# Kernel optimization log

Hardware: AMD Instinct MI355X
Metric: run time of the kernel (lower is better)

## Reference

```python
import jax, jax.numpy as jnp
import numpy as np

HIDDEN_DIM = 512
RADIUS = 128


def rel_pos_indexes(seq_len_q: int, seq_len_k: int, radius: int):
    # (i - j) clamped to [-radius, radius], shifted to [0, 2*radius]
    i = jnp.arange(seq_len_k)[None, :]   # [1, Sk]
    j = jnp.arange(seq_len_q)[:, None]   # [Sq, 1]
    return jnp.clip(i - j, -radius, radius) + radius  # [Sq, Sk] int


def setup_inputs() -> dict:
    key = jax.random.key(0)
    kq, kk, kv, ke = jax.random.split(key, 4)
    B, Sq, Sk, d = 4, 2048, 2048, HIDDEN_DIM
    Q = jax.random.normal(kq, (B, Sq, d), dtype=jnp.float32)
    K = jax.random.normal(kk, (B, Sk, d), dtype=jnp.float32)
    V = jax.random.normal(kv, (B, Sk, d), dtype=jnp.float32)
    # learned relative-position embedding table: (2R+1, d)
    rel_embeds = jax.random.normal(ke, (2 * RADIUS + 1, d), dtype=jnp.float32)
    return {"Q": Q, "K": K, "V": V, "rel_embeds": rel_embeds}


def reference(Q, K, V, rel_embeds):
    B, Sq, d = Q.shape
    Sk = K.shape[1]
    normalizer = jnp.asarray(d ** 0.5, dtype=Q.dtype)
    # content scores: [B, Sq, Sk]
    energy = jnp.einsum('bqd,bkd->bqk', Q, K)
    # relative scores: Q against the (2R+1) relative embeddings -> [B, Sq, 2R+1]
    Q_rel = jnp.einsum('bqd,rd->bqr', Q, rel_embeds)
    idx = rel_pos_indexes(Sq, Sk, RADIUS)  # [Sq, Sk]
    # gather along last dim per query row (same index map for every batch)
    rel_shift = jnp.take_along_axis(Q_rel, idx[None, :, :].repeat(B, axis=0), axis=2)
    energy = (energy + rel_shift) / normalizer
    attn = jax.nn.softmax(energy, axis=2)
    Z = jnp.einsum('bqk,bkd->bqd', attn, V)
    return attn, Z
```

## Files before the change

### kernel.cpp

```cpp
#include <hip/hip_runtime.h>

#define BATCH 4
#define SQL 2048
#define SKL 2048
#define DIM 512
#define NR 257
#define NRP 288
#define RAD 128

typedef __bf16 bf16x8 __attribute__((ext_vector_type(8)));
typedef float f32x4 __attribute__((ext_vector_type(4)));
typedef unsigned short u16;
typedef u16 u16x4 __attribute__((ext_vector_type(4)));
typedef u16 u16x8 __attribute__((ext_vector_type(8)));

__device__ inline u16 f2bf(float x) {
  union { float f; unsigned u; } v; v.f = x;
  unsigned r = v.u + 0x7FFF + ((v.u >> 16) & 1);
  return (u16)(r >> 16);
}

__device__ inline void glds16(const u16* g, const u16* l) {
  __builtin_amdgcn_global_load_lds(
      (const __attribute__((address_space(1))) void*)g,
      (__attribute__((address_space(3))) void*)l, 16, 0, 0);
}

__global__ __launch_bounds__(256) void prep_mem_kernel(const float* __restrict__ Q,
                                                       const float* __restrict__ K,
                                                       const float* __restrict__ V,
                                                       const float* __restrict__ rel,
                                                       u16x4* __restrict__ Qb,
                                                       u16x4* __restrict__ Kb,
                                                       u16* __restrict__ relb,
                                                       u16* __restrict__ Vt) {
  __shared__ float tile[32][33];
  int bid = blockIdx.x, tid = threadIdx.x;
  if (bid < 8192) {
    const f32x4* src = (bid < 4096) ? (const f32x4*)Q : (const f32x4*)K;
    u16x4* dst = (bid < 4096) ? Qb : Kb;
    int i = (bid & 4095) * 256 + tid;
    f32x4 f = src[i];
    u16x4 o;
#pragma unroll
    for (int e = 0; e < 4; e++) o[e] = f2bf(f[e]);
    dst[i] = o;
  } else if (bid < 8768) {
    int i = (bid - 8192) * 256 + tid;
    int r = i >> 9;
    relb[i] = (r < NR) ? f2bf(rel[i]) : (u16)0;
  } else {
    int t = bid - 8768;
    int b = t >> 10, rem = t & 1023;
    int k0 = (rem & 63) * 32, d0 = (rem >> 6) * 32;
    int tx = tid & 31, ty = tid >> 5;
#pragma unroll
    for (int r = 0; r < 4; r++)
      tile[ty + r * 8][tx] = V[((long)b * SKL + k0 + ty + r * 8) * DIM + d0 + tx];
    __syncthreads();
#pragma unroll
    for (int r = 0; r < 4; r++)
      Vt[((long)b * DIM + d0 + ty + r * 8) * SKL + k0 + tx] = f2bf(tile[tx][ty + r * 8]);
  }
}

__global__ __launch_bounds__(256) void qrel_kernel(const u16* __restrict__ Qb,
                                                   const u16* __restrict__ relb,
                                                   float* __restrict__ Qrel) {
  int tid = threadIdx.x;
  int wave = tid >> 6, lane = tid & 63;
  int m0 = blockIdx.x * 64 + wave * 16;
  int j0 = blockIdx.y * 2;
  int fr = lane & 15, fk = (lane >> 4) * 8;
  f32x4 acc[2] = {};
  const u16* qrow = Qb + (long)(m0 + fr) * DIM + fk;
  const u16* r0 = relb + (long)(j0 * 16 + fr) * DIM + fk;
  const u16* r1 = r0 + 16 * DIM;
  for (int k0 = 0; k0 < DIM; k0 += 32) {
    bf16x8 a = *(const bf16x8*)(qrow + k0);
    bf16x8 b0 = *(const bf16x8*)(r0 + k0);
    bf16x8 b1 = *(const bf16x8*)(r1 + k0);
    acc[0] = __builtin_amdgcn_mfma_f32_16x16x32_bf16(a, b0, acc[0], 0, 0, 0);
    acc[1] = __builtin_amdgcn_mfma_f32_16x16x32_bf16(a, b1, acc[1], 0, 0, 0);
  }
  int cr = (lane >> 4) * 4, cc = lane & 15;
#pragma unroll
  for (int t = 0; t < 2; t++)
#pragma unroll
    for (int r = 0; r < 4; r++)
      Qrel[(long)(m0 + cr + r) * NRP + (j0 + t) * 16 + cc] = acc[t][r];
}

__global__ __launch_bounds__(256) void energy_kernel(const u16* __restrict__ Qb,
                                                     const u16* __restrict__ Kb,
                                                     u16* __restrict__ S) {
  int b = blockIdx.z;
  int m0 = blockIdx.y * 128;
  int n0 = blockIdx.x * 128;
  const u16* A = Qb + (long)b * SQL * DIM;
  const u16* Bp = Kb + (long)b * SKL * DIM;
  __shared__ u16 As[128 * 32];
  __shared__ u16 Bs[128 * 32];
  int tid = threadIdx.x;
  int wave = tid >> 6, lane = tid & 63;
  int wm = (wave >> 1) * 64, wn = (wave & 1) * 64;
  int fr = lane & 15, fk = (lane >> 4) * 8;
  int srow = wave * 32 + (lane >> 2);
  int scol = (lane & 3) * 8;
  f32x4 acc[4][4] = {};
  for (int k0 = 0; k0 < DIM; k0 += 32) {
    __syncthreads();
    glds16(A + (long)(m0 + srow) * DIM + k0 + scol, As + (wave * 2 + 0) * 512);
    glds16(A + (long)(m0 + srow + 16) * DIM + k0 + scol, As + (wave * 2 + 1) * 512);
    glds16(Bp + (long)(n0 + srow) * DIM + k0 + scol, Bs + (wave * 2 + 0) * 512);
    glds16(Bp + (long)(n0 + srow + 16) * DIM + k0 + scol, Bs + (wave * 2 + 1) * 512);
    __syncthreads();
    bf16x8 af[4], bfr[4];
#pragma unroll
    for (int i = 0; i < 4; i++) af[i] = *(const bf16x8*)(As + (wm + i * 16 + fr) * 32 + fk);
#pragma unroll
    for (int j = 0; j < 4; j++) bfr[j] = *(const bf16x8*)(Bs + (wn + j * 16 + fr) * 32 + fk);
#pragma unroll
    for (int i = 0; i < 4; i++)
#pragma unroll
      for (int j = 0; j < 4; j++)
        acc[i][j] = __builtin_amdgcn_mfma_f32_16x16x32_bf16(af[i], bfr[j], acc[i][j], 0, 0, 0);
  }
  const float inv_norm = 0.04419417382415922f;
  int cr = (lane >> 4) * 4, cc = lane & 15;
#pragma unroll
  for (int i = 0; i < 4; i++) {
#pragma unroll
    for (int r = 0; r < 4; r++) {
      int q = m0 + wm + i * 16 + cr + r;
      u16* sr = S + ((long)b * SQL + q) * SKL;
#pragma unroll
      for (int j = 0; j < 4; j++)
        sr[n0 + wn + j * 16 + cc] = f2bf(acc[i][j][r] * inv_norm);
    }
  }
}

__global__ __launch_bounds__(256) void softmax_kernel(u16* __restrict__ S,
                                                      const float* __restrict__ Qrel,
                                                      float* __restrict__ attn) {
  long row = blockIdx.x;
  int q = (int)(row & (SQL - 1));
  u16* srow = S + row * SKL;
  float* arow = attn + row * SKL;
  int tid = threadIdx.x;
  int wave = tid >> 6, lane = tid & 63;
  __shared__ float qlds[NR];
  __shared__ float red[4];
  const float inv_norm = 0.04419417382415922f;
  const float* qr = Qrel + row * NRP;
  qlds[tid] = qr[tid] * inv_norm;
  if (tid == 0) qlds[256] = qr[256] * inv_norm;
  bf16x8 v = *(const bf16x8*)(srow + tid * 8);
  __syncthreads();
  float f[8];
  int kb = tid * 8 - q + RAD;
#pragma unroll
  for (int e = 0; e < 8; e++) {
    int idx = kb + e;
    idx = idx < 0 ? 0 : (idx > 2 * RAD ? 2 * RAD : idx);
    f[e] = (float)v[e] + qlds[idx];
  }
  float m = -1e30f;
#pragma unroll
  for (int e = 0; e < 8; e++) m = fmaxf(m, f[e]);
  for (int o = 32; o > 0; o >>= 1) m = fmaxf(m, __shfl_xor(m, o));
  if (lane == 0) red[wave] = m;
  __syncthreads();
  m = fmaxf(fmaxf(red[0], red[1]), fmaxf(red[2], red[3]));
  __syncthreads();
  float s = 0.0f;
  float e8[8];
#pragma unroll
  for (int e = 0; e < 8; e++) { e8[e] = __expf(f[e] - m); s += e8[e]; }
  for (int o = 32; o > 0; o >>= 1) s += __shfl_xor(s, o);
  if (lane == 0) red[wave] = s;
  __syncthreads();
  s = red[0] + red[1] + red[2] + red[3];
  float inv = 1.0f / s;
  f32x4 o0, o1;
  u16x8 pb;
#pragma unroll
  for (int e = 0; e < 4; e++) {
    float p = e8[e] * inv;
    o0[e] = p; pb[e] = f2bf(p);
  }
#pragma unroll
  for (int e = 0; e < 4; e++) {
    float p = e8[e + 4] * inv;
    o1[e] = p; pb[e + 4] = f2bf(p);
  }
  *(f32x4*)(arow + tid * 8) = o0;
  *(f32x4*)(arow + tid * 8 + 4) = o1;
  *(u16x8*)(srow + tid * 8) = pb;
}

__global__ __launch_bounds__(256) void z_kernel(const u16* __restrict__ S,
                                                const u16* __restrict__ Vt,
                                                float* __restrict__ Z) {
  int b = blockIdx.z;
  int m0 = blockIdx.y * 64;
  int n0 = blockIdx.x * 128;
  const u16* A = S + (long)b * SQL * SKL;
  const u16* Bp = Vt + (long)b * DIM * SKL;
  __shared__ u16 As[64 * 32];
  __shared__ u16 Bs[128 * 32];
  int tid = threadIdx.x;
  int wave = tid >> 6, lane = tid & 63;
  int wm = (wave >> 1) * 32, wn = (wave & 1) * 64;
  int fr = lane & 15, fk = (lane >> 4) * 8;
  int srowA = wave * 16 + (lane >> 2);
  int srowB = wave * 32 + (lane >> 2);
  int scol = (lane & 3) * 8;
  f32x4 acc[2][4] = {};
  for (int k0 = 0; k0 < SKL; k0 += 32) {
    __syncthreads();
    glds16(A + (long)(m0 + srowA) * SKL + k0 + scol, As + wave * 512);
    glds16(Bp + (long)(n0 + srowB) * SKL + k0 + scol, Bs + (wave * 2 + 0) * 512);
    glds16(Bp + (long)(n0 + srowB + 16) * SKL + k0 + scol, Bs + (wave * 2 + 1) * 512);
    __syncthreads();
    bf16x8 af[2], bfr[4];
#pragma unroll
    for (int i = 0; i < 2; i++) af[i] = *(const bf16x8*)(As + (wm + i * 16 + fr) * 32 + fk);
#pragma unroll
    for (int j = 0; j < 4; j++) bfr[j] = *(const bf16x8*)(Bs + (wn + j * 16 + fr) * 32 + fk);
#pragma unroll
    for (int i = 0; i < 2; i++)
#pragma unroll
      for (int j = 0; j < 4; j++)
        acc[i][j] = __builtin_amdgcn_mfma_f32_16x16x32_bf16(af[i], bfr[j], acc[i][j], 0, 0, 0);
  }
  int cr = (lane >> 4) * 4, cc = lane & 15;
#pragma unroll
  for (int i = 0; i < 2; i++)
#pragma unroll
    for (int r = 0; r < 4; r++) {
      int q = m0 + wm + i * 16 + cr + r;
      float* zrow = Z + ((long)b * SQL + q) * DIM;
#pragma unroll
      for (int j = 0; j < 4; j++)
        zrow[n0 + wn + j * 16 + cc] = acc[i][j][r];
    }
}


extern "C" void kernel_launch(void* const* d_in, const int* in_sizes, int n_in,
                              void* d_out, int out_size, void* d_ws, size_t ws_size,
                              hipStream_t stream) {
  const float* Q = (const float*)d_in[0];
  const float* K = (const float*)d_in[1];
  const float* V = (const float*)d_in[2];
  const float* rel = (const float*)d_in[3];
  float* attn = (float*)d_out;
  float* Z = attn + (long)BATCH * SQL * SKL;

  char* ws = (char*)d_ws;
  u16* Qb   = (u16*)ws;
  u16* Kb   = (u16*)(ws + 8388608);
  u16* Vt   = (u16*)(ws + 16777216);
  u16* relb = (u16*)(ws + 25165824);
  float* Qrel = (float*)(ws + 25460736);
  u16* S    = (u16*)(ws + 34897920);

  prep_mem_kernel<<<12864, 256, 0, stream>>>(Q, K, V, rel, (u16x4*)Qb, (u16x4*)Kb, relb, Vt);
  qrel_kernel<<<dim3(128, 9), 256, 0, stream>>>(Qb, relb, Qrel);
  energy_kernel<<<dim3(16, 16, BATCH), 256, 0, stream>>>(Qb, Kb, S);
  softmax_kernel<<<8192, 256, 0, stream>>>(S, Qrel, attn);
  z_kernel<<<dim3(4, 32, BATCH), 256, 0, stream>>>(S, Vt, Z);
}
```

Baseline: 239.8 us.

## Double-buffer LDS with XOR-swizzled K=64 tiles in energy and Z GEMMs

Both bf16 GEMM kernels (QK^T energy and attn·V) now stage K-tiles of 64 instead of 32 into two LDS buffers. The next tile is loaded with global_load_lds while the current one is computed, which cuts the syncs per K step and overlaps memory latency with MFMA work. Column chunks are XOR-swizzled by row to avoid LDS bank conflicts on the fragment reads. The cost is much more LDS per block (64KB for energy, 48KB for Z), which may reduce occupancy.

```diff
diff --git a/kernel.cpp b/kernel.cpp
--- a/kernel.cpp
+++ b/kernel.cpp
@@ -99,33 +99,63 @@
   int n0 = blockIdx.x * 128;
   const u16* A = Qb + (long)b * SQL * DIM;
   const u16* Bp = Kb + (long)b * SKL * DIM;
-  __shared__ u16 As[128 * 32];
-  __shared__ u16 Bs[128 * 32];
+  __shared__ u16 lds[32768];
+  u16* As0 = lds;          u16* Bs0 = lds + 8192;
+  u16* As1 = lds + 16384;  u16* Bs1 = lds + 24576;
   int tid = threadIdx.x;
   int wave = tid >> 6, lane = tid & 63;
   int wm = (wave >> 1) * 64, wn = (wave & 1) * 64;
-  int fr = lane & 15, fk = (lane >> 4) * 8;
-  int srow = wave * 32 + (lane >> 2);
-  int scol = (lane & 3) * 8;
+  int fr = lane & 15, g = lane >> 4;
+  int srow = lane >> 3;
+  int scol = ((lane & 7) ^ srow) * 8;
   f32x4 acc[4][4] = {};
-  for (int k0 = 0; k0 < DIM; k0 += 32) {
+
+  auto stage = [&](u16* dA, u16* dB, int k0) {
+#pragma unroll
+    for (int c = 0; c < 4; c++) {
+      int r = wave * 32 + c * 8;
+      glds16(A + (long)(m0 + r + srow) * DIM + k0 + scol, dA + r * 64);
+      glds16(Bp + (long)(n0 + r + srow) * DIM + k0 + scol, dB + r * 64);
+    }
+  };
+  auto compute = [&](const u16* Asb, const u16* Bsb) {
+#pragma unroll
+    for (int s = 0; s < 2; s++) {
+      bf16x8 af[4], bfv[4];
+#pragma unroll
+      for (int i = 0; i < 4; i++) {
+        int row = wm + i * 16 + fr;
+        int cb = (s * 64 + g * 16) ^ ((row & 7) << 4);
+        af[i] = *(const bf16x8*)(Asb + row * 64 + (cb >> 1));
+      }
+#pragma unroll
+      for (int j = 0; j < 4; j++) {
+        int row = wn + j * 16 + fr;
+        int cb = (s * 64 + g * 16) ^ ((row & 7) << 4);
+        bfv[j] = *(const bf16x8*)(Bsb + row * 64 + (cb >> 1));
+      }
+#pragma unroll
+      for (int i = 0; i < 4; i++)
+#pragma unroll
+        for (int j = 0; j < 4; j++)
+          acc[i][j] = __builtin_amdgcn_mfma_f32_16x16x32_bf16(af[i], bfv[j], acc[i][j], 0, 0, 0);
+    }
+  };
+
+  const int NT = DIM / 64;
+  stage(As0, Bs0, 0);
+  __syncthreads();
+  for (int t = 0; t < NT; t += 2) {
+    if (t + 1 < NT) stage(As1, Bs1, (t + 1) * 64);
+    compute(As0, Bs0);
     __syncthreads();
-    glds16(A + (long)(m0 + srow) * DIM + k0 + scol, As + (wave * 2 + 0) * 512);
-    glds16(A + (long)(m0 + srow + 16) * DIM + k0 + scol, As + (wave * 2 + 1) * 512);
-    glds16(Bp + (long)(n0 + srow) * DIM + k0 + scol, Bs + (wave * 2 + 0) * 512);
-    glds16(Bp + (long)(n0 + srow + 16) * DIM + k0 + scol, Bs + (wave * 2 + 1) * 512);
-    __syncthreads();
-    bf16x8 af[4], bfr[4];
-#pragma unroll
-    for (int i = 0; i < 4; i++) af[i] = *(const bf16x8*)(As + (wm + i * 16 + fr) * 32 + fk);
-#pragma unroll
-    for (int j = 0; j < 4; j++) bfr[j] = *(const bf16x8*)(Bs + (wn + j * 16 + fr) * 32 + fk);
-#pragma unroll
-    for (int i = 0; i < 4; i++)
-#pragma unroll
-      for (int j = 0; j < 4; j++)
-        acc[i][j] = __builtin_amdgcn_mfma_f32_16x16x32_bf16(af[i], bfr[j], acc[i][j], 0, 0, 0);
-  }
+    if (t + 1 < NT) {
+      if (t + 2 < NT) stage(As0, Bs0, (t + 2) * 64);
+      compute(As1, Bs1);
+      __syncthreads();
+    }
+  }
+
   const float inv_norm = 0.04419417382415922f;
   int cr = (lane >> 4) * 4, cc = lane & 15;
 #pragma unroll
@@ -208,33 +238,67 @@
   int n0 = blockIdx.x * 128;
   const u16* A = S + (long)b * SQL * SKL;
   const u16* Bp = Vt + (long)b * DIM * SKL;
-  __shared__ u16 As[64 * 32];
-  __shared__ u16 Bs[128 * 32];
+  __shared__ u16 lds[24576];
+  u16* As0 = lds;          u16* Bs0 = lds + 4096;
+  u16* As1 = lds + 12288;  u16* Bs1 = lds + 16384;
   int tid = threadIdx.x;
   int wave = tid >> 6, lane = tid & 63;
   int wm = (wave >> 1) * 32, wn = (wave & 1) * 64;
-  int fr = lane & 15, fk = (lane >> 4) * 8;
-  int srowA = wave * 16 + (lane >> 2);
-  int srowB = wave * 32 + (lane >> 2);
-  int scol = (lane & 3) * 8;
+  int fr = lane & 15, g = lane >> 4;
+  int srow = lane >> 3;
+  int scol = ((lane & 7) ^ srow) * 8;
   f32x4 acc[2][4] = {};
-  for (int k0 = 0; k0 < SKL; k0 += 32) {
+
+  auto stage = [&](u16* dA, u16* dB, int k0) {
+#pragma unroll
+    for (int c = 0; c < 2; c++) {
+      int r = wave * 16 + c * 8;
+      glds16(A + (long)(m0 + r + srow) * SKL + k0 + scol, dA + r * 64);
+    }
+#pragma unroll
+    for (int c = 0; c < 4; c++) {
+      int r = wave * 32 + c * 8;
+      glds16(Bp + (long)(n0 + r + srow) * SKL + k0 + scol, dB + r * 64);
+    }
+  };
+  auto compute = [&](const u16* Asb, const u16* Bsb) {
+#pragma unroll
+    for (int s = 0; s < 2; s++) {
+      bf16x8 af[2], bfv[4];
+#pragma unroll
+      for (int i = 0; i < 2; i++) {
+        int row = wm + i * 16 + fr;
+        int cb = (s * 64 + g * 16) ^ ((row & 7) << 4);
+        af[i] = *(const bf16x8*)(Asb + row * 64 + (cb >> 1));
+      }
+#pragma unroll
+      for (int j = 0; j < 4; j++) {
+        int row = wn + j * 16 + fr;
+        int cb = (s * 64 + g * 16) ^ ((row & 7) << 4);
+        bfv[j] = *(const bf16x8*)(Bsb + row * 64 + (cb >> 1));
+      }
+#pragma unroll
+      for (int i = 0; i < 2; i++)
+#pragma unroll
+        for (int j = 0; j < 4; j++)
+          acc[i][j] = __builtin_amdgcn_mfma_f32_16x16x32_bf16(af[i], bfv[j], acc[i][j], 0, 0, 0);
+    }
+  };
+
+  const int NT = SKL / 64;
+  stage(As0, Bs0, 0);
+  __syncthreads();
+  for (int t = 0; t < NT; t += 2) {
+    if (t + 1 < NT) stage(As1, Bs1, (t + 1) * 64);
+    compute(As0, Bs0);
     __syncthreads();
-    glds16(A + (long)(m0 + srowA) * SKL + k0 + scol, As + wave * 512);
-    glds16(Bp + (long)(n0 + srowB) * SKL + k0 + scol, Bs + (wave * 2 + 0) * 512);
-    glds16(Bp + (long)(n0 + srowB + 16) * SKL + k0 + scol, Bs + (wave * 2 + 1) * 512);
-    __syncthreads();
-    bf16x8 af[2], bfr[4];
-#pragma unroll
-    for (int i = 0; i < 2; i++) af[i] = *(const bf16x8*)(As + (wm + i * 16 + fr) * 32 + fk);
-#pragma unroll
-    for (int j = 0; j < 4; j++) bfr[j] = *(const bf16x8*)(Bs + (wn + j * 16 + fr) * 32 + fk);
-#pragma unroll
-    for (int i = 0; i < 2; i++)
-#pragma unroll
-      for (int j = 0; j < 4; j++)
-        acc[i][j] = __builtin_amdgcn_mfma_f32_16x16x32_bf16(af[i], bfr[j], acc[i][j], 0, 0, 0);
-  }
+    if (t + 1 < NT) {
+      if (t + 2 < NT) stage(As0, Bs0, (t + 2) * 64);
+      compute(As1, Bs1);
+      __syncthreads();
+    }
+  }
+
   int cr = (lane >> 4) * 4, cc = lane & 15;
 #pragma unroll
   for (int i = 0; i < 2; i++)
```

Result: faster. 232.7 us (-3.0%).

## Fuse energy, softmax and PV GEMM into one kernel with LDS-resident score rows

Applied to the files above, without the earlier changes.

Replaces the separate energy GEMM, softmax and Z GEMM kernels with one fused kernel. Each 512-thread block handles 16 query rows and keeps the full 16x2048 bf16 score/probability tile in swizzled LDS, so the intermediate S matrix no longer goes to global memory. The cost is much smaller tiles: each wave streams K and V fragments straight from global memory with no LDS sharing. This gives low data reuse, a grid of only 512 blocks, and a large LDS footprint (about 96KB) that limits occupancy.

```diff
diff --git a/kernel.cpp b/kernel.cpp
--- a/kernel.cpp
+++ b/kernel.cpp
@@ -25,6 +25,9 @@
       (const __attribute__((address_space(1))) void*)g,
       (__attribute__((address_space(3))) void*)l, 16, 0, 0);
 }
+
+#define PSWZ(row, cb) (((row) << 12) + ((cb) ^ (((row) & 7) << 4)))
+#define QSWZ(row, cb) (((row) << 10) + ((cb) ^ (((row) & 7) << 4)))
 
 __global__ __launch_bounds__(256) void prep_mem_kernel(const float* __restrict__ Q,
                                                        const float* __restrict__ K,
@@ -91,161 +94,145 @@
       Qrel[(long)(m0 + cr + r) * NRP + (j0 + t) * 16 + cc] = acc[t][r];
 }
 
-__global__ __launch_bounds__(256) void energy_kernel(const u16* __restrict__ Qb,
-                                                     const u16* __restrict__ Kb,
-                                                     u16* __restrict__ S) {
-  int b = blockIdx.z;
-  int m0 = blockIdx.y * 128;
-  int n0 = blockIdx.x * 128;
-  const u16* A = Qb + (long)b * SQL * DIM;
-  const u16* Bp = Kb + (long)b * SKL * DIM;
-  __shared__ u16 As[128 * 32];
-  __shared__ u16 Bs[128 * 32];
+__global__ __launch_bounds__(512, 2) void attn_fused_kernel(const u16* __restrict__ Qb,
+                                                            const u16* __restrict__ Kb,
+                                                            const u16* __restrict__ Vt,
+                                                            const float* __restrict__ Qrel,
+                                                            float* __restrict__ attn,
+                                                            float* __restrict__ Z) {
+  __shared__ u16 P[16 * 2048];
+  __shared__ u16 Qs[16 * 512];
+  __shared__ float qlds[16][264];
+
+  int b = blockIdx.y;
+  int m0 = blockIdx.x * 16;
   int tid = threadIdx.x;
   int wave = tid >> 6, lane = tid & 63;
-  int wm = (wave >> 1) * 64, wn = (wave & 1) * 64;
   int fr = lane & 15, fk = (lane >> 4) * 8;
-  int srow = wave * 32 + (lane >> 2);
-  int scol = (lane & 3) * 8;
-  f32x4 acc[4][4] = {};
-  for (int k0 = 0; k0 < DIM; k0 += 32) {
-    __syncthreads();
-    glds16(A + (long)(m0 + srow) * DIM + k0 + scol, As + (wave * 2 + 0) * 512);
-    glds16(A + (long)(m0 + srow + 16) * DIM + k0 + scol, As + (wave * 2 + 1) * 512);
-    glds16(Bp + (long)(n0 + srow) * DIM + k0 + scol, Bs + (wave * 2 + 0) * 512);
-    glds16(Bp + (long)(n0 + srow + 16) * DIM + k0 + scol, Bs + (wave * 2 + 1) * 512);
-    __syncthreads();
-    bf16x8 af[4], bfr[4];
-#pragma unroll
-    for (int i = 0; i < 4; i++) af[i] = *(const bf16x8*)(As + (wm + i * 16 + fr) * 32 + fk);
-#pragma unroll
-    for (int j = 0; j < 4; j++) bfr[j] = *(const bf16x8*)(Bs + (wn + j * 16 + fr) * 32 + fk);
-#pragma unroll
-    for (int i = 0; i < 4; i++)
-#pragma unroll
-      for (int j = 0; j < 4; j++)
-        acc[i][j] = __builtin_amdgcn_mfma_f32_16x16x32_bf16(af[i], bfr[j], acc[i][j], 0, 0, 0);
-  }
+  int cr = (lane >> 4) * 4, cc = lane & 15;
   const float inv_norm = 0.04419417382415922f;
-  int cr = (lane >> 4) * 4, cc = lane & 15;
-#pragma unroll
-  for (int i = 0; i < 4; i++) {
-#pragma unroll
-    for (int r = 0; r < 4; r++) {
-      int q = m0 + wm + i * 16 + cr + r;
-      u16* sr = S + ((long)b * SQL + q) * SKL;
-#pragma unroll
-      for (int j = 0; j < 4; j++)
-        sr[n0 + wn + j * 16 + cc] = f2bf(acc[i][j][r] * inv_norm);
-    }
-  }
-}
-
-__global__ __launch_bounds__(256) void softmax_kernel(u16* __restrict__ S,
-                                                      const float* __restrict__ Qrel,
-                                                      float* __restrict__ attn) {
-  long row = blockIdx.x;
-  int q = (int)(row & (SQL - 1));
-  u16* srow = S + row * SKL;
-  float* arow = attn + row * SKL;
-  int tid = threadIdx.x;
-  int wave = tid >> 6, lane = tid & 63;
-  __shared__ float qlds[NR];
-  __shared__ float red[4];
-  const float inv_norm = 0.04419417382415922f;
-  const float* qr = Qrel + row * NRP;
-  qlds[tid] = qr[tid] * inv_norm;
-  if (tid == 0) qlds[256] = qr[256] * inv_norm;
-  bf16x8 v = *(const bf16x8*)(srow + tid * 8);
+
+  const u16* Qb_b = Qb + (long)b * SQL * DIM;
+  const u16* Kb_b = Kb + (long)b * SKL * DIM;
+  const u16* Vt_b = Vt + (long)b * DIM * SKL;
+
+  {
+    int row = tid >> 5, c0 = (tid & 31) * 16;
+    const u16* src = Qb_b + (long)(m0 + row) * DIM + c0;
+    bf16x8 v0 = *(const bf16x8*)(src);
+    bf16x8 v1 = *(const bf16x8*)(src + 8);
+    *(bf16x8*)(Qs + (QSWZ(row, c0 * 2) >> 1)) = v0;
+    *(bf16x8*)(Qs + (QSWZ(row, c0 * 2 + 16) >> 1)) = v1;
+    const float* qr = Qrel + ((long)b * SQL + m0 + row) * NRP;
+    for (int j = tid & 31; j < NR; j += 32) qlds[row][j] = qr[j] * inv_norm;
+  }
   __syncthreads();
-  float f[8];
-  int kb = tid * 8 - q + RAD;
-#pragma unroll
-  for (int e = 0; e < 8; e++) {
-    int idx = kb + e;
-    idx = idx < 0 ? 0 : (idx > 2 * RAD ? 2 * RAD : idx);
-    f[e] = (float)v[e] + qlds[idx];
-  }
-  float m = -1e30f;
-#pragma unroll
-  for (int e = 0; e < 8; e++) m = fmaxf(m, f[e]);
-  for (int o = 32; o > 0; o >>= 1) m = fmaxf(m, __shfl_xor(m, o));
-  if (lane == 0) red[wave] = m;
+
+  {
+    int n0 = wave * 256;
+    const u16* Kbw = Kb_b + (long)(n0 + fr) * DIM + fk;
+    f32x4 acc[16] = {};
+#pragma unroll 4
+    for (int k0 = 0; k0 < DIM; k0 += 32) {
+      bf16x8 a = *(const bf16x8*)(Qs + (QSWZ(fr, (k0 + fk) * 2) >> 1));
+      bf16x8 bb[8];
+#pragma unroll
+      for (int j = 0; j < 8; j++) bb[j] = *(const bf16x8*)(Kbw + (long)j * 16 * DIM + k0);
+#pragma unroll
+      for (int j = 0; j < 8; j++)
+        acc[j] = __builtin_amdgcn_mfma_f32_16x16x32_bf16(a, bb[j], acc[j], 0, 0, 0);
+#pragma unroll
+      for (int j = 0; j < 8; j++) bb[j] = *(const bf16x8*)(Kbw + (long)(j + 8) * 16 * DIM + k0);
+#pragma unroll
+      for (int j = 0; j < 8; j++)
+        acc[j + 8] = __builtin_amdgcn_mfma_f32_16x16x32_bf16(a, bb[j], acc[j + 8], 0, 0, 0);
+    }
+#pragma unroll
+    for (int j = 0; j < 16; j++) {
+      int col = n0 + j * 16 + cc;
+#pragma unroll
+      for (int r = 0; r < 4; r++) {
+        int row = cr + r;
+        P[PSWZ(row, col * 2) >> 1] = f2bf(acc[j][r] * inv_norm);
+      }
+    }
+  }
   __syncthreads();
-  m = fmaxf(fmaxf(red[0], red[1]), fmaxf(red[2], red[3]));
+
+  {
+    int s = tid & 31, prow = tid >> 5;
+    int q = m0 + prow;
+    float* arow = attn + ((long)b * SQL + q) * SKL;
+    float mx = -1e30f;
+#pragma unroll
+    for (int c = 0; c < 16; c++) {
+      int col = s * 4 + c * 128;
+      u16x4 pv = *(const u16x4*)(P + (PSWZ(prow, col * 2) >> 1));
+#pragma unroll
+      for (int e = 0; e < 4; e++) {
+        int idx = col + e - q + RAD;
+        idx = idx < 0 ? 0 : (idx > 2 * RAD ? 2 * RAD : idx);
+        union { u16 u[2]; float f; } cv; cv.u[0] = 0; cv.u[1] = pv[e];
+        mx = fmaxf(mx, cv.f + qlds[prow][idx]);
+      }
+    }
+#pragma unroll
+    for (int o = 1; o <= 16; o <<= 1) mx = fmaxf(mx, __shfl_xor(mx, o));
+    float sum = 0.0f;
+#pragma unroll
+    for (int c = 0; c < 16; c++) {
+      int col = s * 4 + c * 128;
+      u16x4 pv = *(const u16x4*)(P + (PSWZ(prow, col * 2) >> 1));
+#pragma unroll
+      for (int e = 0; e < 4; e++) {
+        int idx = col + e - q + RAD;
+        idx = idx < 0 ? 0 : (idx > 2 * RAD ? 2 * RAD : idx);
+        union { u16 u[2]; float f; } cv; cv.u[0] = 0; cv.u[1] = pv[e];
+        sum += __expf(cv.f + qlds[prow][idx] - mx);
+      }
+    }
+#pragma unroll
+    for (int o = 1; o <= 16; o <<= 1) sum += __shfl_xor(sum, o);
+    float inv = 1.0f / sum;
+#pragma unroll
+    for (int c = 0; c < 16; c++) {
+      int col = s * 4 + c * 128;
+      u16x4 pv = *(const u16x4*)(P + (PSWZ(prow, col * 2) >> 1));
+      f32x4 o4;
+      u16x4 pb;
+#pragma unroll
+      for (int e = 0; e < 4; e++) {
+        int idx = col + e - q + RAD;
+        idx = idx < 0 ? 0 : (idx > 2 * RAD ? 2 * RAD : idx);
+        union { u16 u[2]; float f; } cv; cv.u[0] = 0; cv.u[1] = pv[e];
+        float p = __expf(cv.f + qlds[prow][idx] - mx) * inv;
+        o4[e] = p; pb[e] = f2bf(p);
+      }
+      *(f32x4*)(arow + col) = o4;
+      *(u16x4*)(P + (PSWZ(prow, col * 2) >> 1)) = pb;
+    }
+  }
   __syncthreads();
-  float s = 0.0f;
-  float e8[8];
-#pragma unroll
-  for (int e = 0; e < 8; e++) { e8[e] = __expf(f[e] - m); s += e8[e]; }
-  for (int o = 32; o > 0; o >>= 1) s += __shfl_xor(s, o);
-  if (lane == 0) red[wave] = s;
-  __syncthreads();
-  s = red[0] + red[1] + red[2] + red[3];
-  float inv = 1.0f / s;
-  f32x4 o0, o1;
-  u16x8 pb;
-#pragma unroll
-  for (int e = 0; e < 4; e++) {
-    float p = e8[e] * inv;
-    o0[e] = p; pb[e] = f2bf(p);
-  }
-#pragma unroll
-  for (int e = 0; e < 4; e++) {
-    float p = e8[e + 4] * inv;
-    o1[e] = p; pb[e + 4] = f2bf(p);
-  }
-  *(f32x4*)(arow + tid * 8) = o0;
-  *(f32x4*)(arow + tid * 8 + 4) = o1;
-  *(u16x8*)(srow + tid * 8) = pb;
-}
-
-__global__ __launch_bounds__(256) void z_kernel(const u16* __restrict__ S,
-                                                const u16* __restrict__ Vt,
-                                                float* __restrict__ Z) {
-  int b = blockIdx.z;
-  int m0 = blockIdx.y * 64;
-  int n0 = blockIdx.x * 128;
-  const u16* A = S + (long)b * SQL * SKL;
-  const u16* Bp = Vt + (long)b * DIM * SKL;
-  __shared__ u16 As[64 * 32];
-  __shared__ u16 Bs[128 * 32];
-  int tid = threadIdx.x;
-  int wave = tid >> 6, lane = tid & 63;
-  int wm = (wave >> 1) * 32, wn = (wave & 1) * 64;
-  int fr = lane & 15, fk = (lane >> 4) * 8;
-  int srowA = wave * 16 + (lane >> 2);
-  int srowB = wave * 32 + (lane >> 2);
-  int scol = (lane & 3) * 8;
-  f32x4 acc[2][4] = {};
-  for (int k0 = 0; k0 < SKL; k0 += 32) {
-    __syncthreads();
-    glds16(A + (long)(m0 + srowA) * SKL + k0 + scol, As + wave * 512);
-    glds16(Bp + (long)(n0 + srowB) * SKL + k0 + scol, Bs + (wave * 2 + 0) * 512);
-    glds16(Bp + (long)(n0 + srowB + 16) * SKL + k0 + scol, Bs + (wave * 2 + 1) * 512);
-    __syncthreads();
-    bf16x8 af[2], bfr[4];
-#pragma unroll
-    for (int i = 0; i < 2; i++) af[i] = *(const bf16x8*)(As + (wm + i * 16 + fr) * 32 + fk);
-#pragma unroll
-    for (int j = 0; j < 4; j++) bfr[j] = *(const bf16x8*)(Bs + (wn + j * 16 + fr) * 32 + fk);
-#pragma unroll
-    for (int i = 0; i < 2; i++)
-#pragma unroll
-      for (int j = 0; j < 4; j++)
-        acc[i][j] = __builtin_amdgcn_mfma_f32_16x16x32_bf16(af[i], bfr[j], acc[i][j], 0, 0, 0);
-  }
-  int cr = (lane >> 4) * 4, cc = lane & 15;
-#pragma unroll
-  for (int i = 0; i < 2; i++)
-#pragma unroll
-    for (int r = 0; r < 4; r++) {
-      int q = m0 + wm + i * 16 + cr + r;
-      float* zrow = Z + ((long)b * SQL + q) * DIM;
-#pragma unroll
-      for (int j = 0; j < 4; j++)
-        zrow[n0 + wn + j * 16 + cc] = acc[i][j][r];
-    }
+
+  {
+    int wn = wave * 64;
+    const u16* Vw = Vt_b + (long)(wn + fr) * SKL + fk;
+    f32x4 acc2[4] = {};
+#pragma unroll 2
+    for (int k0 = 0; k0 < SKL; k0 += 32) {
+      bf16x8 a = *(const bf16x8*)(P + (PSWZ(fr, (k0 + fk) * 2) >> 1));
+#pragma unroll
+      for (int j = 0; j < 4; j++) {
+        bf16x8 bv = *(const bf16x8*)(Vw + (long)j * 16 * SKL + k0);
+        acc2[j] = __builtin_amdgcn_mfma_f32_16x16x32_bf16(a, bv, acc2[j], 0, 0, 0);
+      }
+    }
+#pragma unroll
+    for (int j = 0; j < 4; j++)
+#pragma unroll
+      for (int r = 0; r < 4; r++)
+        Z[((long)b * SQL + m0 + cr + r) * DIM + wn + j * 16 + cc] = acc2[j][r];
+  }
 }
 
 
@@ -265,11 +252,8 @@
   u16* Vt   = (u16*)(ws + 16777216);
   u16* relb = (u16*)(ws + 25165824);
   float* Qrel = (float*)(ws + 25460736);
-  u16* S    = (u16*)(ws + 34897920);
 
   prep_mem_kernel<<<12864, 256, 0, stream>>>(Q, K, V, rel, (u16x4*)Qb, (u16x4*)Kb, relb, Vt);
   qrel_kernel<<<dim3(128, 9), 256, 0, stream>>>(Qb, relb, Qrel);
-  energy_kernel<<<dim3(16, 16, BATCH), 256, 0, stream>>>(Qb, Kb, S);
-  softmax_kernel<<<8192, 256, 0, stream>>>(S, Qrel, attn);
-  z_kernel<<<dim3(4, 32, BATCH), 256, 0, stream>>>(S, Vt, Z);
-}
+  attn_fused_kernel<<<dim3(128, BATCH), 512, 0, stream>>>(Qb, Kb, Vt, Qrel, attn, Z);
+}
```

Measured after the change: 391.4 us. 63.2% more time.
